# Optimization experiments

Hardware: AMD Instinct MI355X
Metric: run time of the kernel (lower is better)

## Reference

```python
import jax, jax.numpy as jnp
import numpy as np

D_MODEL = 1024
N_HEAD = 16
D_K = D_MODEL // N_HEAD


def setup_inputs() -> dict:
    key = jax.random.key(0)
    ks = jax.random.split(key, 11)
    B, S = 4, 2048
    s = 1.0 / np.sqrt(D_MODEL)
    return {
        "q": jax.random.normal(ks[0], (B, S, D_MODEL), jnp.float32),
        "k": jax.random.normal(ks[1], (B, S, D_MODEL), jnp.float32),
        "v": jax.random.normal(ks[2], (B, S, D_MODEL), jnp.float32),
        "w_q": jax.random.normal(ks[3], (D_MODEL, D_MODEL), jnp.float32) * s,
        "b_q": jnp.zeros((D_MODEL,), jnp.float32),
        "w_k": jax.random.normal(ks[4], (D_MODEL, D_MODEL), jnp.float32) * s,
        "b_k": jnp.zeros((D_MODEL,), jnp.float32),
        "w_v": jax.random.normal(ks[5], (D_MODEL, D_MODEL), jnp.float32) * s,
        "b_v": jnp.zeros((D_MODEL,), jnp.float32),
        "w_o": jax.random.normal(ks[6], (D_MODEL, D_MODEL), jnp.float32) * s,
        "b_o": jnp.zeros((D_MODEL,), jnp.float32),
    }


def reference(q, k, v, w_q, b_q, w_k, b_k, w_v, b_v, w_o, b_o):
    B, S, _ = q.shape
    # projections (torch Linear: x @ W^T + b)
    qp = q @ w_q.T + b_q
    kp = k @ w_k.T + b_k
    vp = v @ w_v.T + b_v
    # split heads -> [B, H, S, d_k]
    qh = qp.reshape(B, S, N_HEAD, D_K).transpose(0, 2, 1, 3)
    kh = kp.reshape(B, S, N_HEAD, D_K).transpose(0, 2, 1, 3)
    vh = vp.reshape(B, S, N_HEAD, D_K).transpose(0, 2, 1, 3)
    # scaled dot-product attention
    scores = jnp.einsum("bhqd,bhkd->bhqk", qh, kh) / jnp.sqrt(jnp.float32(D_K)).astype(qh.dtype)
    attn = jax.nn.softmax(scores, axis=-1)
    out = jnp.einsum("bhqk,bhkd->bhqd", attn, vh)
    # merge heads -> [B, S, d_model]
    out = out.transpose(0, 2, 1, 3).reshape(B, S, D_MODEL)
    return out @ w_o.T + b_o
```

## Files before the change

kernel.cpp:

```cpp
#include <hip/hip_runtime.h>
#include <hip/hip_bf16.h>
#include <stdint.h>

#define D_MODEL 1024
#define SEQ     2048
#define NBATCH  4
#define NHEAD   16
#define MROWS   (NBATCH*SEQ)

typedef __attribute__((ext_vector_type(8))) short short8;
typedef __attribute__((ext_vector_type(4))) float floatx4;
typedef __attribute__((ext_vector_type(2))) unsigned int uint2v;

#if __has_builtin(__builtin_amdgcn_exp2f)
#define EXP2(x) __builtin_amdgcn_exp2f(x)
#else
#define EXP2(x) exp2f(x)
#endif

__device__ __forceinline__ unsigned short f2bf(float f) {
  unsigned int x;
  __builtin_memcpy(&x, &f, 4);
  x += 0x7fffu + ((x >> 16) & 1u);
  return (unsigned short)(x >> 16);
}

__device__ __forceinline__ unsigned int pk2(float a, float b) {
  __hip_bfloat162 h = __float22bfloat162_rn(make_float2(a, b));
  unsigned int u;
  __builtin_memcpy(&u, &h, 4);
  return u;
}

__device__ __forceinline__ void gl_lds16(const unsigned short* g, unsigned short* l) {
  __builtin_amdgcn_global_load_lds(
      (const __attribute__((address_space(1))) unsigned int*)g,
      (__attribute__((address_space(3))) unsigned int*)l, 16, 0, 0);
}

__global__ __launch_bounds__(256)
void cvt_all(const float* __restrict__ q, const float* __restrict__ k,
             const float* __restrict__ v, const float* __restrict__ wq,
             const float* __restrict__ wk, const float* __restrict__ wv,
             const float* __restrict__ wo,
             unsigned short* __restrict__ dq, unsigned short* __restrict__ dk,
             unsigned short* __restrict__ dv, unsigned short* __restrict__ dwq,
             unsigned short* __restrict__ dwk, unsigned short* __restrict__ dwv,
             unsigned short* __restrict__ dwo) {
  const unsigned QV4 = (MROWS * D_MODEL) / 4u;
  const unsigned WV4 = (D_MODEL * D_MODEL) / 4u;
  const unsigned total = 3u * QV4 + 4u * WV4;
  for (unsigned i = blockIdx.x * 256u + threadIdx.x; i < total;
       i += gridDim.x * 256u) {
    const float* s;
    unsigned short* d;
    unsigned off;
    if (i < 3u * QV4) {
      const unsigned t = i >> 21;
      off = i & (QV4 - 1u);
      s = (t == 0) ? q : (t == 1) ? k : v;
      d = (t == 0) ? dq : (t == 1) ? dk : dv;
    } else {
      const unsigned j = i - 3u * QV4;
      const unsigned t = j >> 18;
      off = j & (WV4 - 1u);
      s = (t == 0) ? wq : (t == 1) ? wk : (t == 2) ? wv : wo;
      d = (t == 0) ? dwq : (t == 1) ? dwk : (t == 2) ? dwv : dwo;
    }
    const floatx4 f = *(const floatx4*)(s + (size_t)off * 4);
    uint2v u;
    u.x = pk2(f[0], f[1]);
    u.y = pk2(f[2], f[3]);
    *(uint2v*)(d + (size_t)off * 4) = u;
  }
}

template <int OMODE>
__device__ __forceinline__ void gemm_body(const unsigned short* __restrict__ A,
                                          const unsigned short* __restrict__ W,
                                          const float* __restrict__ bias,
                                          void* __restrict__ Y_,
                                          int M, int N, int K, float scale,
                                          unsigned short* As, unsigned short* Bs) {
  const int tid  = threadIdx.x;
  const int lane = tid & 63;
  const int w    = tid >> 6;
  const int rho  = lane & 15;
  const int quad = lane >> 4;
  const int ntile = N >> 7;
  const int cpx = gridDim.x >> 3;
  const int wg  = (blockIdx.x & 7) * cpx + (blockIdx.x >> 3);
  const int bx = wg % ntile;
  const int by = wg / ntile;
  const int tm = by << 7, tn = bx << 7;
  const int wrow = (w >> 1) << 6;
  const int wcol = (w & 1) << 6;

  const int lrow = lane >> 3;
  const int g    = ((lane & 7) - lrow) & 7;
  const unsigned short* gA = A + (size_t)(tm + w * 32 + lrow) * K + g * 8;
  const unsigned short* gB = W + (size_t)(tn + w * 32 + lrow) * K + g * 8;

  floatx4 acc[4][4] = {};

#define GSTAGE(buf, kk)                                                        \
  _Pragma("unroll") for (int c = 0; c < 4; c++) {                              \
    gl_lds16(gA + (size_t)c * 8 * K + (kk), &As[(buf)*8192 + (w*256 + c*64)*8]); \
    gl_lds16(gB + (size_t)c * 8 * K + (kk), &Bs[(buf)*8192 + (w*256 + c*64)*8]); \
  }

  GSTAGE(0, 0);
  __syncthreads();

  for (int kk = 0; kk < K; kk += 64) {
    const int cur = (kk >> 6) & 1;
    if (kk + 64 < K) { GSTAGE(cur ^ 1, kk + 64); }
    const unsigned short* as = &As[cur * 8192];
    const unsigned short* bs = &Bs[cur * 8192];
#pragma unroll
    for (int h = 0; h < 2; h++) {
      const int kp = (quad + rho + h * 4) & 7;
      short8 af[4], bf4[4];
#pragma unroll
      for (int i = 0; i < 4; i++)
        af[i] = *(const short8*)&as[(wrow + i * 16 + rho) * 64 + kp * 8];
#pragma unroll
      for (int j = 0; j < 4; j++)
        bf4[j] = *(const short8*)&bs[(wcol + j * 16 + rho) * 64 + kp * 8];
#pragma unroll
      for (int i = 0; i < 4; i++)
#pragma unroll
        for (int j = 0; j < 4; j++)
          acc[i][j] = __builtin_amdgcn_mfma_f32_16x16x32_bf16(af[i], bf4[j],
                                                              acc[i][j], 0, 0, 0);
    }
    __syncthreads();
  }
#undef GSTAGE

  float bj[4];
#pragma unroll
  for (int j = 0; j < 4; j++) bj[j] = bias[tn + wcol + j * 16 + rho];
#pragma unroll
  for (int i = 0; i < 4; i++) {
    const int grow = tm + wrow + i * 16 + (quad << 2);
#pragma unroll
    for (int j = 0; j < 4; j++) {
      const int gcol = tn + wcol + j * 16 + rho;
#pragma unroll
      for (int r = 0; r < 4; r++) {
        const float val = (acc[i][j][r] + bj[j]) * scale;
        if (OMODE == 1)
          ((float*)Y_)[(size_t)(grow + r) * N + gcol] = val;
        else
          ((unsigned short*)Y_)[(size_t)(grow + r) * N + gcol] = f2bf(val);
      }
    }
  }
}

template <int OMODE>
__global__ __launch_bounds__(256, 2)
void gemm_one(const unsigned short* __restrict__ A,
              const unsigned short* __restrict__ W,
              const float* __restrict__ bias, void* __restrict__ Y_,
              int M, int N, int K, float scale) {
  __shared__ __attribute__((aligned(16))) unsigned short As[2 * 128 * 64];
  __shared__ __attribute__((aligned(16))) unsigned short Bs[2 * 128 * 64];
  gemm_body<OMODE>(A, W, bias, Y_, M, N, K, scale, As, Bs);
}

__global__ __launch_bounds__(256, 2)
void gemm_qkv(const unsigned short* __restrict__ qb, const unsigned short* __restrict__ wqb,
              const float* __restrict__ bq, unsigned short* __restrict__ Qp,
              const unsigned short* __restrict__ kb, const unsigned short* __restrict__ wkb,
              const float* __restrict__ bk, unsigned short* __restrict__ Kp,
              const unsigned short* __restrict__ vb, const unsigned short* __restrict__ wvb,
              const float* __restrict__ bv, unsigned short* __restrict__ Vp,
              float qscale) {
  __shared__ __attribute__((aligned(16))) unsigned short As[2 * 128 * 64];
  __shared__ __attribute__((aligned(16))) unsigned short Bs[2 * 128 * 64];
  const int y = blockIdx.y;
  const unsigned short* A = (y == 0) ? qb : (y == 1) ? kb : vb;
  const unsigned short* W = (y == 0) ? wqb : (y == 1) ? wkb : wvb;
  const float* bias       = (y == 0) ? bq : (y == 1) ? bk : bv;
  unsigned short* Y       = (y == 0) ? Qp : (y == 1) ? Kp : Vp;
  const float scale = (y == 0) ? qscale : 1.0f;
  gemm_body<0>(A, W, bias, Y, MROWS, D_MODEL, D_MODEL, scale, As, Bs);
}

__global__ __launch_bounds__(256, 2)
void attn_fused(const unsigned short* __restrict__ Qp,
                const unsigned short* __restrict__ Kp,
                const unsigned short* __restrict__ Vp,
                unsigned short* __restrict__ AO) {
  __shared__ unsigned short Ks[2][64*64];
  __shared__ unsigned short Vt[2][64*72];
  __shared__ unsigned short Pl[4][64*72];

  const int tid  = threadIdx.x;
  const int w    = tid >> 6;
  const int lane = tid & 63;
  const int rho  = lane & 15;
  const int quad = lane >> 4;

  const int qt = blockIdx.x & 7;
  const int bh = blockIdx.x >> 3;
  const int b  = bh >> 4;
  const int h  = bh & 15;
  const size_t base = (size_t)b*SEQ*D_MODEL + h*64;
  const unsigned short* Qb = Qp + base;
  const unsigned short* Kb = Kp + base;
  const unsigned short* Vb = Vp + base;

  const int q0 = qt*256 + w*64;

  short8 aq[4][2];
#pragma unroll
  for (int u = 0; u < 4; u++) {
    const unsigned short* qr = Qb + (size_t)(q0 + u*16 + rho)*D_MODEL + quad*8;
    aq[u][0] = *(const short8*)qr;
    aq[u][1] = *(const short8*)(qr + 32);
  }

  float lsum[4][4] = {};
  floatx4 oacc[4][4] = {};

  const int vkey = lane;
  const int vkap = ((vkey & 15) << 2) | (vkey >> 4);

  const int s0 = w*64 + lane;
  const int k0key = s0 >> 3, k0g = ((s0 & 7) - k0key) & 7;
  const int s1 = 256 + w*64 + lane;
  const int k1key = s1 >> 3, k1g = ((s1 & 7) - k1key) & 7;

  const int kp0 = (quad + rho) & 7;
  const int kp1 = (kp0 + 4) & 7;

  gl_lds16(Kb + (size_t)k0key*D_MODEL + k0g*8, &Ks[0][(w*64)*8]);
  gl_lds16(Kb + (size_t)k1key*D_MODEL + k1g*8, &Ks[0][(256 + w*64)*8]);

  for (int kb = 0; kb < SEQ; kb += 64) {
    const int bi = (kb >> 6) & 1;

    {
      const unsigned short* vr = Vb + (size_t)(kb + vkey)*D_MODEL + w*16;
      const short8 v0 = *(const short8*)vr;
      const short8 v1 = *(const short8*)(vr + 8);
      unsigned short* dst = &Vt[bi][w*16*72 + vkap];
#pragma unroll
      for (int e = 0; e < 8; e++) dst[e*72] = (unsigned short)v0[e];
#pragma unroll
      for (int e = 0; e < 8; e++) dst[(8 + e)*72] = (unsigned short)v1[e];
    }
    __syncthreads();

    if (kb + 64 < SEQ) {
      unsigned short* kn = &Ks[bi ^ 1][0];
      gl_lds16(Kb + (size_t)(kb + 64 + k0key)*D_MODEL + k0g*8, kn + (w*64)*8);
      gl_lds16(Kb + (size_t)(kb + 64 + k1key)*D_MODEL + k1g*8, kn + (256 + w*64)*8);
    }

    const unsigned short* ks = &Ks[bi][0];
    floatx4 sc[4][4];
#pragma unroll
    for (int gk = 0; gk < 4; gk++) {
      const int key = gk*16 + rho;
      const short8 kf0 = *(const short8*)(ks + (key*8 + kp0)*8);
      const short8 kf1 = *(const short8*)(ks + (key*8 + kp1)*8);
#pragma unroll
      for (int u = 0; u < 4; u++) {
        floatx4 t = {0.f, 0.f, 0.f, 0.f};
        t = __builtin_amdgcn_mfma_f32_16x16x32_bf16(aq[u][0], kf0, t, 0, 0, 0);
        t = __builtin_amdgcn_mfma_f32_16x16x32_bf16(aq[u][1], kf1, t, 0, 0, 0);
        sc[u][gk] = t;
      }
    }

#pragma unroll
    for (int u = 0; u < 4; u++)
#pragma unroll
      for (int r = 0; r < 4; r++) {
        const float e0 = EXP2(sc[u][0][r]);
        const float e1 = EXP2(sc[u][1][r]);
        const float e2 = EXP2(sc[u][2][r]);
        const float e3 = EXP2(sc[u][3][r]);
        lsum[u][r] += (e0 + e1) + (e2 + e3);
        const unsigned int lo = pk2(e0, e1);
        const unsigned int hi = pk2(e2, e3);
        const int row = u*16 + (quad << 2) + r;
        *(uint2v*)&Pl[w][row*72 + rho*4] = (uint2v){lo, hi};
      }

    short8 bv[4][2];
#pragma unroll
    for (int c = 0; c < 4; c++) {
      bv[c][0] = *(const short8*)&Vt[bi][(c*16 + rho)*72 + quad*8];
      bv[c][1] = *(const short8*)&Vt[bi][(c*16 + rho)*72 + 32 + quad*8];
    }
#pragma unroll
    for (int u = 0; u < 4; u++) {
      const short8 ap0 = *(const short8*)&Pl[w][(u*16 + rho)*72 + quad*8];
      const short8 ap1 = *(const short8*)&Pl[w][(u*16 + rho)*72 + 32 + quad*8];
#pragma unroll
      for (int c = 0; c < 4; c++) {
        oacc[u][c] = __builtin_amdgcn_mfma_f32_16x16x32_bf16(ap0, bv[c][0], oacc[u][c], 0, 0, 0);
        oacc[u][c] = __builtin_amdgcn_mfma_f32_16x16x32_bf16(ap1, bv[c][1], oacc[u][c], 0, 0, 0);
      }
    }
  }

#pragma unroll
  for (int d = 1; d < 16; d <<= 1)
#pragma unroll
    for (int u = 0; u < 4; u++)
#pragma unroll
      for (int r = 0; r < 4; r++) lsum[u][r] += __shfl_xor(lsum[u][r], d);

#pragma unroll
  for (int u = 0; u < 4; u++) {
    float inv[4];
#pragma unroll
    for (int r = 0; r < 4; r++) inv[r] = 1.0f / lsum[u][r];
#pragma unroll
    for (int c = 0; c < 4; c++)
#pragma unroll
      for (int r = 0; r < 4; r++)
        AO[base + (size_t)(q0 + u*16 + (quad << 2) + r)*D_MODEL + c*16 + rho] =
            f2bf(oacc[u][c][r] * inv[r]);
  }
}

extern "C" void kernel_launch(void* const* d_in, const int* in_sizes, int n_in,
                              void* d_out, int out_size, void* d_ws, size_t ws_size,
                              hipStream_t stream) {
  const float* q  = (const float*)d_in[0];
  const float* k  = (const float*)d_in[1];
  const float* v  = (const float*)d_in[2];
  const float* wq = (const float*)d_in[3];
  const float* bq = (const float*)d_in[4];
  const float* wk = (const float*)d_in[5];
  const float* bk = (const float*)d_in[6];
  const float* wv = (const float*)d_in[7];
  const float* bv = (const float*)d_in[8];
  const float* wo = (const float*)d_in[9];
  const float* bo = (const float*)d_in[10];
  float* out = (float*)d_out;

  unsigned short* Qp  = (unsigned short*)d_ws;
  unsigned short* Kp  = Qp + (size_t)MROWS*D_MODEL;
  unsigned short* Vp  = Kp + (size_t)MROWS*D_MODEL;
  unsigned short* AO  = Vp + (size_t)MROWS*D_MODEL;
  unsigned short* qb  = AO + (size_t)MROWS*D_MODEL;
  unsigned short* kb  = qb + (size_t)MROWS*D_MODEL;
  unsigned short* vb  = kb + (size_t)MROWS*D_MODEL;
  unsigned short* wqb = vb + (size_t)MROWS*D_MODEL;
  unsigned short* wkb = wqb + (size_t)D_MODEL*D_MODEL;
  unsigned short* wvb = wkb + (size_t)D_MODEL*D_MODEL;
  unsigned short* wob = wvb + (size_t)D_MODEL*D_MODEL;

  const float qscale = 0.125f * 1.4426950408889634f;

  const dim3 blk(256);
  cvt_all<<<dim3(2048), blk, 0, stream>>>(q, k, v, wq, wk, wv, wo,
                                          qb, kb, vb, wqb, wkb, wvb, wob);

  gemm_qkv<<<dim3((D_MODEL/128) * (MROWS/128), 3), blk, 0, stream>>>(
      qb, wqb, bq, Qp, kb, wkb, bk, Kp, vb, wvb, bv, Vp, qscale);

  attn_fused<<<dim3(NBATCH*NHEAD*(SEQ/256)), blk, 0, stream>>>(Qp, Kp, Vp, AO);

  gemm_one<1><<<dim3((D_MODEL/128) * (MROWS/128)), blk, 0, stream>>>(
      AO, wob, bo, out, MROWS, D_MODEL, D_MODEL, 1.0f);
}
```

Measured before the change: 337.7 us.

## Keep softmax probabilities in registers via transposed QK MFMA, prefetch V into registers

Swaps the MFMA operand order in the score computation so each lane holds scores already laid out as the A operand of the PV MFMA. This removes the per-wave LDS round trip for the probability tile, and V's LDS transpose layout is permuted to match the new key ordering. The main loop is unrolled by two and V global loads are issued one tile ahead into registers, so their latency overlaps compute. Block index mapping also changes so consecutive blocks walk different heads and batches rather than query tiles. The row sum becomes per-lane, reduced with cross-quad shuffles and redistributed at the end. This costs more registers for the prefetched V and the packed probabilities, which may hurt occupancy.

```diff
diff --git a/kernel.cpp b/kernel.cpp
--- a/kernel.cpp
+++ b/kernel.cpp
@@ -189,6 +189,59 @@
   gemm_body<0>(A, W, bias, Y, MROWS, D_MODEL, D_MODEL, scale, As, Bs);
 }
 
+__device__ __forceinline__ void attn_step(const unsigned short* __restrict__ ks,
+                                          const unsigned short* __restrict__ vt,
+                                          const short8 (&aq)[4][2],
+                                          float (&lsum)[4], floatx4 (&oacc)[4][4],
+                                          int rho, int quad, int kp0, int kp1) {
+  floatx4 sc[4][4];
+#pragma unroll
+  for (int gk = 0; gk < 4; gk++) {
+    const int key = gk*16 + rho;
+    const short8 kf0 = *(const short8*)(ks + (key*8 + kp0)*8);
+    const short8 kf1 = *(const short8*)(ks + (key*8 + kp1)*8);
+#pragma unroll
+    for (int u = 0; u < 4; u++) {
+      floatx4 t = {0.f, 0.f, 0.f, 0.f};
+      t = __builtin_amdgcn_mfma_f32_16x16x32_bf16(kf0, aq[u][0], t, 0, 0, 0);
+      t = __builtin_amdgcn_mfma_f32_16x16x32_bf16(kf1, aq[u][1], t, 0, 0, 0);
+      sc[u][gk] = t;
+    }
+  }
+  short8 pa0[4], pa1[4];
+#pragma unroll
+  for (int u = 0; u < 4; u++) {
+    float E[4][4];
+#pragma unroll
+    for (int gk = 0; gk < 4; gk++)
+#pragma unroll
+      for (int r = 0; r < 4; r++) E[gk][r] = EXP2(sc[u][gk][r]);
+    float s01 = 0.f, s23 = 0.f;
+#pragma unroll
+    for (int r = 0; r < 4; r++) { s01 += E[0][r] + E[1][r]; s23 += E[2][r] + E[3][r]; }
+    lsum[u] += s01 + s23;
+    union { short8 s; unsigned int w4[4]; } a0, a1;
+    a0.w4[0] = pk2(E[0][0], E[0][1]); a0.w4[1] = pk2(E[0][2], E[0][3]);
+    a0.w4[2] = pk2(E[1][0], E[1][1]); a0.w4[3] = pk2(E[1][2], E[1][3]);
+    a1.w4[0] = pk2(E[2][0], E[2][1]); a1.w4[1] = pk2(E[2][2], E[2][3]);
+    a1.w4[2] = pk2(E[3][0], E[3][1]); a1.w4[3] = pk2(E[3][2], E[3][3]);
+    pa0[u] = a0.s; pa1[u] = a1.s;
+  }
+  short8 bv0[4], bv1[4];
+#pragma unroll
+  for (int c = 0; c < 4; c++) {
+    bv0[c] = *(const short8*)&vt[(c*16 + rho)*72 + quad*8];
+    bv1[c] = *(const short8*)&vt[(c*16 + rho)*72 + 32 + quad*8];
+  }
+#pragma unroll
+  for (int u = 0; u < 4; u++)
+#pragma unroll
+    for (int c = 0; c < 4; c++) {
+      oacc[u][c] = __builtin_amdgcn_mfma_f32_16x16x32_bf16(pa0[u], bv0[c], oacc[u][c], 0, 0, 0);
+      oacc[u][c] = __builtin_amdgcn_mfma_f32_16x16x32_bf16(pa1[u], bv1[c], oacc[u][c], 0, 0, 0);
+    }
+}
+
 __global__ __launch_bounds__(256, 2)
 void attn_fused(const unsigned short* __restrict__ Qp,
                 const unsigned short* __restrict__ Kp,
@@ -196,7 +249,6 @@
                 unsigned short* __restrict__ AO) {
   __shared__ unsigned short Ks[2][64*64];
   __shared__ unsigned short Vt[2][64*72];
-  __shared__ unsigned short Pl[4][64*72];
 
   const int tid  = threadIdx.x;
   const int w    = tid >> 6;
@@ -204,8 +256,8 @@
   const int rho  = lane & 15;
   const int quad = lane >> 4;
 
-  const int qt = blockIdx.x & 7;
-  const int bh = blockIdx.x >> 3;
+  const int qt = blockIdx.x >> 6;
+  const int bh = blockIdx.x & 63;
   const int b  = bh >> 4;
   const int h  = bh & 15;
   const size_t base = (size_t)b*SEQ*D_MODEL + h*64;
@@ -223,11 +275,11 @@
     aq[u][1] = *(const short8*)(qr + 32);
   }
 
-  float lsum[4][4] = {};
+  float lsum[4] = {};
   floatx4 oacc[4][4] = {};
 
-  const int vkey = lane;
-  const int vkap = ((vkey & 15) << 2) | (vkey >> 4);
+  const int vkap = ((lane >> 2) & 3) * 8 + ((lane >> 4) & 1) * 4 + (lane & 3)
+                 + (lane >> 5) * 32;
 
   const int s0 = w*64 + lane;
   const int k0key = s0 >> 3, k0g = ((s0 & 7) - k0key) & 7;
@@ -237,91 +289,52 @@
   const int kp0 = (quad + rho) & 7;
   const int kp1 = (kp0 + 4) & 7;
 
-  gl_lds16(Kb + (size_t)k0key*D_MODEL + k0g*8, &Ks[0][(w*64)*8]);
-  gl_lds16(Kb + (size_t)k1key*D_MODEL + k1g*8, &Ks[0][(256 + w*64)*8]);
-
-  for (int kb = 0; kb < SEQ; kb += 64) {
-    const int bi = (kb >> 6) & 1;
-
-    {
-      const unsigned short* vr = Vb + (size_t)(kb + vkey)*D_MODEL + w*16;
-      const short8 v0 = *(const short8*)vr;
-      const short8 v1 = *(const short8*)(vr + 8);
-      unsigned short* dst = &Vt[bi][w*16*72 + vkap];
-#pragma unroll
-      for (int e = 0; e < 8; e++) dst[e*72] = (unsigned short)v0[e];
-#pragma unroll
-      for (int e = 0; e < 8; e++) dst[(8 + e)*72] = (unsigned short)v1[e];
-    }
+#define VLOAD(v0r, v1r, kbase)                                                 \
+  { const unsigned short* vr = Vb + (size_t)((kbase) + lane)*D_MODEL + w*16;   \
+    v0r = *(const short8*)vr; v1r = *(const short8*)(vr + 8); }
+#define VWRITE(buf, v0r, v1r)                                                  \
+  { unsigned short* dst = &Vt[buf][w*16*72 + vkap];                            \
+    _Pragma("unroll") for (int e = 0; e < 8; e++) dst[e*72] = (unsigned short)v0r[e]; \
+    _Pragma("unroll") for (int e = 0; e < 8; e++) dst[(8+e)*72] = (unsigned short)v1r[e]; }
+#define KSTAGE(buf, kbase)                                                     \
+  { gl_lds16(Kb + (size_t)((kbase) + k0key)*D_MODEL + k0g*8, &Ks[buf][(w*64)*8]);      \
+    gl_lds16(Kb + (size_t)((kbase) + k1key)*D_MODEL + k1g*8, &Ks[buf][(256 + w*64)*8]); }
+
+  short8 vA0, vA1, vB0, vB1;
+  VLOAD(vA0, vA1, 0);
+  KSTAGE(0, 0);
+
+  for (int kb = 0; kb < SEQ; kb += 128) {
+    VWRITE(0, vA0, vA1);
     __syncthreads();
-
-    if (kb + 64 < SEQ) {
-      unsigned short* kn = &Ks[bi ^ 1][0];
-      gl_lds16(Kb + (size_t)(kb + 64 + k0key)*D_MODEL + k0g*8, kn + (w*64)*8);
-      gl_lds16(Kb + (size_t)(kb + 64 + k1key)*D_MODEL + k1g*8, kn + (256 + w*64)*8);
-    }
-
-    const unsigned short* ks = &Ks[bi][0];
-    floatx4 sc[4][4];
-#pragma unroll
-    for (int gk = 0; gk < 4; gk++) {
-      const int key = gk*16 + rho;
-      const short8 kf0 = *(const short8*)(ks + (key*8 + kp0)*8);
-      const short8 kf1 = *(const short8*)(ks + (key*8 + kp1)*8);
-#pragma unroll
-      for (int u = 0; u < 4; u++) {
-        floatx4 t = {0.f, 0.f, 0.f, 0.f};
-        t = __builtin_amdgcn_mfma_f32_16x16x32_bf16(aq[u][0], kf0, t, 0, 0, 0);
-        t = __builtin_amdgcn_mfma_f32_16x16x32_bf16(aq[u][1], kf1, t, 0, 0, 0);
-        sc[u][gk] = t;
-      }
-    }
-
-#pragma unroll
-    for (int u = 0; u < 4; u++)
-#pragma unroll
-      for (int r = 0; r < 4; r++) {
-        const float e0 = EXP2(sc[u][0][r]);
-        const float e1 = EXP2(sc[u][1][r]);
-        const float e2 = EXP2(sc[u][2][r]);
-        const float e3 = EXP2(sc[u][3][r]);
-        lsum[u][r] += (e0 + e1) + (e2 + e3);
-        const unsigned int lo = pk2(e0, e1);
-        const unsigned int hi = pk2(e2, e3);
-        const int row = u*16 + (quad << 2) + r;
-        *(uint2v*)&Pl[w][row*72 + rho*4] = (uint2v){lo, hi};
-      }
-
-    short8 bv[4][2];
-#pragma unroll
-    for (int c = 0; c < 4; c++) {
-      bv[c][0] = *(const short8*)&Vt[bi][(c*16 + rho)*72 + quad*8];
-      bv[c][1] = *(const short8*)&Vt[bi][(c*16 + rho)*72 + 32 + quad*8];
-    }
-#pragma unroll
-    for (int u = 0; u < 4; u++) {
-      const short8 ap0 = *(const short8*)&Pl[w][(u*16 + rho)*72 + quad*8];
-      const short8 ap1 = *(const short8*)&Pl[w][(u*16 + rho)*72 + 32 + quad*8];
-#pragma unroll
-      for (int c = 0; c < 4; c++) {
-        oacc[u][c] = __builtin_amdgcn_mfma_f32_16x16x32_bf16(ap0, bv[c][0], oacc[u][c], 0, 0, 0);
-        oacc[u][c] = __builtin_amdgcn_mfma_f32_16x16x32_bf16(ap1, bv[c][1], oacc[u][c], 0, 0, 0);
-      }
-    }
-  }
-
-#pragma unroll
-  for (int d = 1; d < 16; d <<= 1)
-#pragma unroll
-    for (int u = 0; u < 4; u++)
-#pragma unroll
-      for (int r = 0; r < 4; r++) lsum[u][r] += __shfl_xor(lsum[u][r], d);
+    VLOAD(vB0, vB1, kb + 64);
+    KSTAGE(1, kb + 64);
+    attn_step(&Ks[0][0], &Vt[0][0], aq, lsum, oacc, rho, quad, kp0, kp1);
+
+    VWRITE(1, vB0, vB1);
+    __syncthreads();
+    if (kb + 128 < SEQ) {
+      VLOAD(vA0, vA1, kb + 128);
+      KSTAGE(0, kb + 128);
+    }
+    attn_step(&Ks[1][0], &Vt[1][0], aq, lsum, oacc, rho, quad, kp0, kp1);
+  }
+#undef VLOAD
+#undef VWRITE
+#undef KSTAGE
+
+#pragma unroll
+  for (int u = 0; u < 4; u++) {
+    lsum[u] += __shfl_xor(lsum[u], 16);
+    lsum[u] += __shfl_xor(lsum[u], 32);
+  }
 
 #pragma unroll
   for (int u = 0; u < 4; u++) {
     float inv[4];
 #pragma unroll
-    for (int r = 0; r < 4; r++) inv[r] = 1.0f / lsum[u][r];
+    for (int r = 0; r < 4; r++)
+      inv[r] = 1.0f / __shfl(lsum[u], quad * 4 + r, 64);
 #pragma unroll
     for (int c = 0; c < 4; c++)
 #pragma unroll
```

After: 314.7 us. 6.8% less time.
